# Kernel tuning notes

Measured on AMD Instinct MI355X. Metric: run time of the kernel, lower is better.

Reference implementation:

```python
import jax, jax.numpy as jnp
import numpy as np

B, D, U = 256, 2048, 2048  # batch, input_dim, units
EPS = 1e-8


def setup_inputs() -> dict:
    key = jax.random.key(0)
    ks = jax.random.split(key, 20)
    sd = 1.0 / np.sqrt(D)
    su = 1.0 / np.sqrt(U)
    inp = {
        'x': jax.random.normal(ks[0], (B, D), jnp.float32),
        'h_prev': jax.random.normal(ks[1], (B, U), jnp.float32),
        'c_prev': jax.random.normal(ks[2], (B, U), jnp.float32),
        'n_prev': jax.random.uniform(ks[3], (B, U), jnp.float32),
        'm_prev': jax.random.normal(ks[4], (B, U), jnp.float32),
        # input-to-gate weights (Dense with bias), keras layout [in, out]
        'Wz': jax.random.normal(ks[5], (D, U), jnp.float32) * sd,
        'Wi': jax.random.normal(ks[6], (D, U), jnp.float32) * sd,
        'Wf': jax.random.normal(ks[7], (D, U), jnp.float32) * sd,
        'Wo': jax.random.normal(ks[8], (D, U), jnp.float32) * sd,
        'bz': jnp.zeros((U,), jnp.float32),
        'bi': jnp.zeros((U,), jnp.float32),
        'bf': jnp.zeros((U,), jnp.float32),
        'bo': jnp.zeros((U,), jnp.float32),
        # recurrent weights (Dense without bias)
        'Uz': jax.random.normal(ks[9], (U, U), jnp.float32) * su,
        'Ui': jax.random.normal(ks[10], (U, U), jnp.float32) * su,
        'Uf': jax.random.normal(ks[11], (U, U), jnp.float32) * su,
        'Uo': jax.random.normal(ks[12], (U, U), jnp.float32) * su,
    }
    return inp


def reference(x, h_prev, c_prev, n_prev, m_prev,
              Wz, Wi, Wf, Wo, bz, bi, bf, bo, Uz, Ui, Uf, Uo):
    # fuse the 8 small GEMMs into 2 wide GEMMs (same math, gates split after)
    W = jnp.concatenate([Wz, Wi, Wf, Wo], axis=1)      # [D, 4U]
    Uc = jnp.concatenate([Uz, Ui, Uf, Uo], axis=1)     # [U, 4U]
    b = jnp.concatenate([bz, bi, bf, bo], axis=0)      # [4U]
    pre = x @ W + h_prev @ Uc + b                      # [B, 4U]
    z_tilde, i_tilde, f_tilde, o_tilde = jnp.split(pre, 4, axis=1)

    # exponential-gate stabilization (forget_gate_type='exponential')
    m_t = jnp.maximum(i_tilde + m_prev, i_tilde)
    i_t = jnp.exp(i_tilde - m_t)
    f_t = jnp.exp(f_tilde + m_prev - m_t)

    o_t = jax.nn.sigmoid(o_tilde)
    z_t = jnp.tanh(z_tilde)

    c_t = f_t * c_prev + i_t * z_t
    n_t = f_t * n_prev + i_t
    h_t = o_t * (c_t / (n_t + EPS))
    return jnp.stack([h_t, c_t, n_t, m_t], axis=0)  # [4, B, U]
```

## Files before the change

### kernel.cpp

```cpp
#include <hip/hip_runtime.h>
#include <cstdint>
#include <cstddef>

#define B_   256
#define D_   2048
#define U_   2048
#define NTOT 8192
#define BN   64
#define BK   64
#define KC   2048
#define ITERS (KC / BK)

typedef _Float16 half8 __attribute__((ext_vector_type(8)));
typedef float floatx16 __attribute__((ext_vector_type(16)));

__global__ __launch_bounds__(256) void prep_kernel(
    const float* __restrict__ x, const float* __restrict__ h,
    _Float16* __restrict__ Ahi)
{
    int gid   = blockIdx.x * 256 + threadIdx.x;
    int chunk = gid >> 8;
    int row   = gid & 255;
    int col0  = chunk * 8;
    const float* src = (col0 < D_) ? (x + row * D_ + col0)
                                   : (h + row * U_ + (col0 - D_));
    float4 v0 = *(const float4*)(src);
    float4 v1 = *(const float4*)(src + 4);
    float v[8] = {v0.x, v0.y, v0.z, v0.w, v1.x, v1.y, v1.z, v1.w};
    half8 hi;
#pragma unroll
    for (int i = 0; i < 8; ++i) hi[i] = (_Float16)v[i];
    *(half8*)(Ahi + (chunk * 256 + row) * 8) = hi;
}

__global__ __launch_bounds__(512, 2) void gemm_kernel(
    const _Float16* __restrict__ Ahi,
    const float* __restrict__ Wz, const float* __restrict__ Wi,
    const float* __restrict__ Wf, const float* __restrict__ Wo,
    const float* __restrict__ Uz, const float* __restrict__ Ui,
    const float* __restrict__ Uf, const float* __restrict__ Uo,
    float* __restrict__ P)
{
    __shared__ __align__(16) _Float16 sA[2][8 * 256 * 8];
    __shared__ __align__(16) _Float16 sB[2][BK * BN];

    const int t    = threadIdx.x;
    const int w    = t >> 6;
    const int lane = t & 63;
    const int lg   = lane >> 5;
    const int lm   = lane & 31;
    const int wm   = w >> 1;
    const int wn   = w & 1;

    const int nblk = blockIdx.x;
    const int ks   = blockIdx.y;
    const int n0   = nblk * BN;
    const int g    = n0 >> 11;
    const int c0   = n0 & (U_ - 1);

    const float* wsel[8] = {Wz, Wi, Wf, Wo, Uz, Ui, Uf, Uo};
    const float* Bm = wsel[ks * 4 + g];
    const int chunk0 = ks * 256;

    const _Float16* Ag = Ahi + (size_t)chunk0 * 2048
                             + (size_t)(w * 4) * 512 + (size_t)lane * 8;

    const float* Bg = Bm + (size_t)(w * 8) * U_ + c0 + lane;
    const int swb = (lane * 128 + w * 16) ^ ((lane & 7) << 4);

    const int aoff = lg * 4096 + (wm * 64 + lm) * 16;

    floatx16 acc0 = {}, acc1 = {};
    float rb0[8], rb1[8];

#define ISSUE_A(tt, buf)                                                      \
    {                                                                         \
        _Pragma("unroll")                                                     \
        for (int i = 0; i < 4; ++i)                                           \
            __builtin_amdgcn_global_load_lds(                                 \
                (const __attribute__((address_space(1))) void*)(              \
                    Ag + (size_t)(tt) * 16384 + i * 512),                     \
                (__attribute__((address_space(3))) void*)(                    \
                    (char*)&sA[buf][0] + (w * 4 + i) * 1024 + lane * 16),     \
                16, 0, 0);                                                    \
    }

#define ISSUE_B(tt, rb)                                                       \
    {                                                                         \
        _Pragma("unroll")                                                     \
        for (int j = 0; j < 8; ++j)                                           \
            rb[j] = Bg[((size_t)(tt) * 64 + j) * U_];                         \
    }

#define WRITE_B(rb, buf)                                                      \
    {                                                                         \
        half8 hv;                                                             \
        _Pragma("unroll")                                                     \
        for (int j = 0; j < 8; ++j) hv[j] = (_Float16)rb[j];                  \
        *(half8*)((char*)&sB[buf][0] + swb) = hv;                             \
    }

#define COMPUTE(cur)                                                          \
    {                                                                         \
        const char* bA = (const char*)&sA[cur][0];                            \
        const char* bB = (const char*)&sB[cur][0];                            \
        half8 af0[4], af1[4], bfr[4];                                         \
        _Pragma("unroll")                                                     \
        for (int kin = 0; kin < 4; ++kin) {                                   \
            af0[kin] = *(const half8*)(bA + aoff + kin * 8192);               \
            af1[kin] = *(const half8*)(bA + aoff + kin * 8192 + 512);         \
            bfr[kin] = *(const half8*)(bB +                                   \
                (((wn * 32 + lm) * 128 + kin * 32 + lg * 16)                  \
                 ^ ((lm & 7) << 4)));                                         \
        }                                                                     \
        __builtin_amdgcn_s_setprio(1);                                        \
        _Pragma("unroll")                                                     \
        for (int kin = 0; kin < 4; ++kin) {                                   \
            acc0 = __builtin_amdgcn_mfma_f32_32x32x16_f16(af0[kin], bfr[kin], acc0, 0, 0, 0); \
            acc1 = __builtin_amdgcn_mfma_f32_32x32x16_f16(af1[kin], bfr[kin], acc1, 0, 0, 0); \
        }                                                                     \
        __builtin_amdgcn_s_setprio(0);                                        \
    }

    ISSUE_A(0, 0);
    ISSUE_B(0, rb1);
    ISSUE_B(1, rb0);
    WRITE_B(rb1, 0);
    asm volatile("s_waitcnt vmcnt(8) lgkmcnt(0)" ::: "memory");
    __builtin_amdgcn_s_barrier();

    for (int tt = 0; tt < ITERS - 2; tt += 2) {
        ISSUE_A(tt + 1, 1);
        ISSUE_B(tt + 2, rb1);
        COMPUTE(0);
        WRITE_B(rb0, 1);
        asm volatile("s_waitcnt vmcnt(8) lgkmcnt(0)" ::: "memory");
        __builtin_amdgcn_s_barrier();

        ISSUE_A(tt + 2, 0);
        ISSUE_B(tt + 3, rb0);
        COMPUTE(1);
        WRITE_B(rb1, 0);
        asm volatile("s_waitcnt vmcnt(8) lgkmcnt(0)" ::: "memory");
        __builtin_amdgcn_s_barrier();
    }

    ISSUE_A(ITERS - 1, 1);
    COMPUTE(0);
    WRITE_B(rb0, 1);
    asm volatile("s_waitcnt vmcnt(0) lgkmcnt(0)" ::: "memory");
    __builtin_amdgcn_s_barrier();
    COMPUTE(1);

#undef ISSUE_A
#undef ISSUE_B
#undef WRITE_B
#undef COMPUTE

    float* Pks = P + (size_t)ks * ((size_t)B_ * NTOT);
    const int ncol = n0 + wn * 32 + lm;
#pragma unroll
    for (int r = 0; r < 16; ++r) {
        int m = wm * 64 + 4 * lg + (r & 3) + 8 * (r >> 2);
        Pks[(size_t)m * NTOT + ncol] = acc0[r];
    }
#pragma unroll
    for (int r = 0; r < 16; ++r) {
        int m = wm * 64 + 32 + 4 * lg + (r & 3) + 8 * (r >> 2);
        Pks[(size_t)m * NTOT + ncol] = acc1[r];
    }
}

__global__ __launch_bounds__(256) void gates_kernel(
    const float* __restrict__ P,
    const float* __restrict__ c_prev, const float* __restrict__ n_prev,
    const float* __restrict__ m_prev,
    const float* __restrict__ bz, const float* __restrict__ bi,
    const float* __restrict__ bf, const float* __restrict__ bo,
    float* __restrict__ out)
{
    const size_t PS = (size_t)B_ * NTOT;
    const int OS = B_ * U_;
    int gid = blockIdx.x * 256 + threadIdx.x;
    int m = gid >> 9;
    int u = (gid & 511) * 4;

    float pre[4][4];
#pragma unroll
    for (int gi = 0; gi < 4; ++gi) {
        const float* base = P + (size_t)m * NTOT + gi * U_ + u;
        float4 s0 = *(const float4*)(base);
        float4 s1 = *(const float4*)(base + PS);
        pre[gi][0] = s0.x + s1.x;
        pre[gi][1] = s0.y + s1.y;
        pre[gi][2] = s0.z + s1.z;
        pre[gi][3] = s0.w + s1.w;
    }
    float4 bzv = *(const float4*)(bz + u);
    float4 biv = *(const float4*)(bi + u);
    float4 bfv = *(const float4*)(bf + u);
    float4 bov = *(const float4*)(bo + u);
    float bza[4] = {bzv.x, bzv.y, bzv.z, bzv.w};
    float bia[4] = {biv.x, biv.y, biv.z, biv.w};
    float bfa[4] = {bfv.x, bfv.y, bfv.z, bfv.w};
    float boa[4] = {bov.x, bov.y, bov.z, bov.w};

    float4 cp4 = *(const float4*)(c_prev + m * U_ + u);
    float4 np4 = *(const float4*)(n_prev + m * U_ + u);
    float4 mp4 = *(const float4*)(m_prev + m * U_ + u);
    float cpa[4] = {cp4.x, cp4.y, cp4.z, cp4.w};
    float npa[4] = {np4.x, np4.y, np4.z, np4.w};
    float mpa[4] = {mp4.x, mp4.y, mp4.z, mp4.w};

    float hr[4], cr[4], nr[4], mr[4];
#pragma unroll
    for (int e = 0; e < 4; ++e) {
        float zt = pre[0][e] + bza[e];
        float it = pre[1][e] + bia[e];
        float ft = pre[2][e] + bfa[e];
        float ot = pre[3][e] + boa[e];
        float mp = mpa[e];
        float m_t = fmaxf(it + mp, it);
        float i_t = expf(it - m_t);
        float f_t = expf(ft + mp - m_t);
        float o_t = 1.0f / (1.0f + expf(-ot));
        float z_t = tanhf(zt);
        float c_t = f_t * cpa[e] + i_t * z_t;
        float n_t = f_t * npa[e] + i_t;
        float h_t = o_t * (c_t / (n_t + 1e-8f));
        hr[e] = h_t; cr[e] = c_t; nr[e] = n_t; mr[e] = m_t;
    }
    float4 hv = {hr[0], hr[1], hr[2], hr[3]};
    float4 cv = {cr[0], cr[1], cr[2], cr[3]};
    float4 nv = {nr[0], nr[1], nr[2], nr[3]};
    float4 mv = {mr[0], mr[1], mr[2], mr[3]};
    *(float4*)(out + 0 * OS + m * U_ + u) = hv;
    *(float4*)(out + 1 * OS + m * U_ + u) = cv;
    *(float4*)(out + 2 * OS + m * U_ + u) = nv;
    *(float4*)(out + 3 * OS + m * U_ + u) = mv;
}

extern "C" void kernel_launch(void* const* d_in, const int* in_sizes, int n_in,
                              void* d_out, int out_size, void* d_ws, size_t ws_size,
                              hipStream_t stream)
{
    const float* x  = (const float*)d_in[0];
    const float* h  = (const float*)d_in[1];
    const float* cp = (const float*)d_in[2];
    const float* np = (const float*)d_in[3];
    const float* mp = (const float*)d_in[4];
    const float* Wz = (const float*)d_in[5];
    const float* Wi = (const float*)d_in[6];
    const float* Wf = (const float*)d_in[7];
    const float* Wo = (const float*)d_in[8];
    const float* bz = (const float*)d_in[9];
    const float* bi = (const float*)d_in[10];
    const float* bf = (const float*)d_in[11];
    const float* bo = (const float*)d_in[12];
    const float* Uz = (const float*)d_in[13];
    const float* Ui = (const float*)d_in[14];
    const float* Uf = (const float*)d_in[15];
    const float* Uo = (const float*)d_in[16];

    float* P = (float*)d_ws;
    _Float16* Ahi = (_Float16*)((char*)d_ws + (size_t)2 * B_ * NTOT * sizeof(float));

    prep_kernel<<<512, 256, 0, stream>>>(x, h, Ahi);
    gemm_kernel<<<dim3(128, 2), 512, 0, stream>>>(Ahi,
        Wz, Wi, Wf, Wo, Uz, Ui, Uf, Uo, P);
    gates_kernel<<<512, 256, 0, stream>>>(P, cp, np, mp, bz, bi, bf, bo,
        (float*)d_out);
}
```

Baseline: 205.9 us.

## Halve GEMM N-tile to 32 with 4-wave blocks and double the grid

Shrinks the GEMM block tile from 64 to 32 output columns and drops to 256 threads (4 waves, each covering 64 rows of M), so the grid doubles to 512 blocks. The goal is to fill more of the CUs than the earlier 256 large blocks could. Each block still loads the full 256xBK A tile per step. A traffic per output column therefore doubles, and each wave issues twice as many A loads into LDS. The B staging index and swizzle are rewritten to match the narrower tile.

```diff
diff --git a/kernel.cpp b/kernel.cpp
--- a/kernel.cpp
+++ b/kernel.cpp
@@ -6,7 +6,7 @@
 #define D_   2048
 #define U_   2048
 #define NTOT 8192
-#define BN   64
+#define BN   32
 #define BK   64
 #define KC   2048
 #define ITERS (KC / BK)
@@ -33,7 +33,7 @@
     *(half8*)(Ahi + (chunk * 256 + row) * 8) = hi;
 }
 
-__global__ __launch_bounds__(512, 2) void gemm_kernel(
+__global__ __launch_bounds__(256, 2) void gemm_kernel(
     const _Float16* __restrict__ Ahi,
     const float* __restrict__ Wz, const float* __restrict__ Wi,
     const float* __restrict__ Wf, const float* __restrict__ Wo,
@@ -49,8 +49,6 @@
     const int lane = t & 63;
     const int lg   = lane >> 5;
     const int lm   = lane & 31;
-    const int wm   = w >> 1;
-    const int wn   = w & 1;
 
     const int nblk = blockIdx.x;
     const int ks   = blockIdx.y;
@@ -63,25 +61,28 @@
     const int chunk0 = ks * 256;
 
     const _Float16* Ag = Ahi + (size_t)chunk0 * 2048
-                             + (size_t)(w * 4) * 512 + (size_t)lane * 8;
-
-    const float* Bg = Bm + (size_t)(w * 8) * U_ + c0 + lane;
-    const int swb = (lane * 128 + w * 16) ^ ((lane & 7) << 4);
-
-    const int aoff = lg * 4096 + (wm * 64 + lm) * 16;
+                             + (size_t)(w * 8) * 512 + (size_t)lane * 8;
+
+    const int scol = t & 31;
+    const int sk0  = (t >> 5) * 8;
+    const float* Bg = Bm + (size_t)sk0 * U_ + c0 + scol;
+    const int swb = scol * 128 + ((sk0 * 2) ^ ((scol & 7) << 4));
+    const int bswz = (lm & 7) << 4;
+
+    const int aoff = lg * 4096 + (w * 64 + lm) * 16;
 
     floatx16 acc0 = {}, acc1 = {};
-    float rb0[8], rb1[8];
+    float rbA[8], rbB[8];
 
 #define ISSUE_A(tt, buf)                                                      \
     {                                                                         \
         _Pragma("unroll")                                                     \
-        for (int i = 0; i < 4; ++i)                                           \
+        for (int i = 0; i < 8; ++i)                                           \
             __builtin_amdgcn_global_load_lds(                                 \
                 (const __attribute__((address_space(1))) void*)(              \
                     Ag + (size_t)(tt) * 16384 + i * 512),                     \
                 (__attribute__((address_space(3))) void*)(                    \
-                    (char*)&sA[buf][0] + (w * 4 + i) * 1024 + lane * 16),     \
+                    (char*)&sA[buf][0] + (w * 8 + i) * 1024 + lane * 16),     \
                 16, 0, 0);                                                    \
     }
 
@@ -109,9 +110,8 @@
         for (int kin = 0; kin < 4; ++kin) {                                   \
             af0[kin] = *(const half8*)(bA + aoff + kin * 8192);               \
             af1[kin] = *(const half8*)(bA + aoff + kin * 8192 + 512);         \
-            bfr[kin] = *(const half8*)(bB +                                   \
-                (((wn * 32 + lm) * 128 + kin * 32 + lg * 16)                  \
-                 ^ ((lm & 7) << 4)));                                         \
+            bfr[kin] = *(const half8*)(bB + lm * 128 +                        \
+                ((kin * 32 + lg * 16) ^ bswz));                               \
         }                                                                     \
         __builtin_amdgcn_s_setprio(1);                                        \
         _Pragma("unroll")                                                     \
@@ -122,32 +122,32 @@
         __builtin_amdgcn_s_setprio(0);                                        \
     }
 
+    ISSUE_B(0, rbA);
     ISSUE_A(0, 0);
-    ISSUE_B(0, rb1);
-    ISSUE_B(1, rb0);
-    WRITE_B(rb1, 0);
+    ISSUE_B(1, rbB);
+    WRITE_B(rbA, 0);
     asm volatile("s_waitcnt vmcnt(8) lgkmcnt(0)" ::: "memory");
     __builtin_amdgcn_s_barrier();
 
     for (int tt = 0; tt < ITERS - 2; tt += 2) {
         ISSUE_A(tt + 1, 1);
-        ISSUE_B(tt + 2, rb1);
+        ISSUE_B(tt + 2, rbA);
         COMPUTE(0);
-        WRITE_B(rb0, 1);
+        WRITE_B(rbB, 1);
         asm volatile("s_waitcnt vmcnt(8) lgkmcnt(0)" ::: "memory");
         __builtin_amdgcn_s_barrier();
 
         ISSUE_A(tt + 2, 0);
-        ISSUE_B(tt + 3, rb0);
+        ISSUE_B(tt + 3, rbB);
         COMPUTE(1);
-        WRITE_B(rb1, 0);
+        WRITE_B(rbA, 0);
         asm volatile("s_waitcnt vmcnt(8) lgkmcnt(0)" ::: "memory");
         __builtin_amdgcn_s_barrier();
     }
 
     ISSUE_A(ITERS - 1, 1);
     COMPUTE(0);
-    WRITE_B(rb0, 1);
+    WRITE_B(rbB, 1);
     asm volatile("s_waitcnt vmcnt(0) lgkmcnt(0)" ::: "memory");
     __builtin_amdgcn_s_barrier();
     COMPUTE(1);
@@ -158,16 +158,15 @@
 #undef COMPUTE
 
     float* Pks = P + (size_t)ks * ((size_t)B_ * NTOT);
-    const int ncol = n0 + wn * 32 + lm;
 #pragma unroll
     for (int r = 0; r < 16; ++r) {
-        int m = wm * 64 + 4 * lg + (r & 3) + 8 * (r >> 2);
-        Pks[(size_t)m * NTOT + ncol] = acc0[r];
+        int m = w * 64 + 4 * lg + (r & 3) + 8 * (r >> 2);
+        Pks[(size_t)m * NTOT + n0 + lm] = acc0[r];
     }
 #pragma unroll
     for (int r = 0; r < 16; ++r) {
-        int m = wm * 64 + 32 + 4 * lg + (r & 3) + 8 * (r >> 2);
-        Pks[(size_t)m * NTOT + ncol] = acc1[r];
+        int m = w * 64 + 32 + 4 * lg + (r & 3) + 8 * (r >> 2);
+        Pks[(size_t)m * NTOT + n0 + lm] = acc1[r];
     }
 }
 
@@ -266,7 +265,7 @@
     _Float16* Ahi = (_Float16*)((char*)d_ws + (size_t)2 * B_ * NTOT * sizeof(float));
 
     prep_kernel<<<512, 256, 0, stream>>>(x, h, Ahi);
-    gemm_kernel<<<dim3(128, 2), 512, 0, stream>>>(Ahi,
+    gemm_kernel<<<dim3(256, 2), 256, 0, stream>>>(Ahi,
         Wz, Wi, Wf, Wo, Uz, Ui, Uf, Uo, P);
     gates_kernel<<<512, 256, 0, stream>>>(P, cp, np, mp, bz, bi, bf, bo,
         (float*)d_out);
```

Result: slower. 213.1 us (+3.5%).
